# Kernel optimization log

Measured on AMD Instinct MI355X. Metric: run time of the kernel, lower is better.

## Reference

```python
import jax, jax.numpy as jnp
import numpy as np

K = 3
KV = K * K * K  # 27 kernel taps


def conv3d(x, w, b):
    # standard Conv3d, stride 1, padding 1 (the offset-predicting conv)
    out = jax.lax.conv_general_dilated(
        x, w, window_strides=(1, 1, 1), padding=[(1, 1), (1, 1), (1, 1)],
        dimension_numbers=('NCDHW', 'OIDHW', 'NCDHW'))
    return out + b[None, :, None, None, None]


def deform_conv3d_hw(x, offset, weight):
    # D3D deformable conv, dimension='HW': per kernel tap (kt,kh,kw) the sample
    # location gets fractional (dh,dw) offsets; t coordinate stays integer.
    B, C, T, H, W = x.shape
    Cout = weight.shape[0]
    off = offset.reshape(B, KV, 2, T, H, W)        # (dh, dw) per tap
    dh, dw = off[:, :, 0], off[:, :, 1]            # [B,KV,T,H,W]
    kt, kh, kw = jnp.meshgrid(jnp.arange(K), jnp.arange(K), jnp.arange(K), indexing='ij')
    kt, kh, kw = kt.reshape(KV), kh.reshape(KV), kw.reshape(KV)
    ti = jnp.arange(T)[None, :, None, None] + (kt - 1)[:, None, None, None]  # [KV,T,1,1] int
    hs = (jnp.arange(H)[None, None, :, None] + (kh - 1)[:, None, None, None]).astype(x.dtype) + dh
    ws = (jnp.arange(W)[None, None, None, :] + (kw - 1)[:, None, None, None]).astype(x.dtype) + dw
    tvalid = (ti >= 0) & (ti < T)                                # [KV,T,1,1]
    tic = jnp.broadcast_to(jnp.clip(ti, 0, T - 1), (KV, T, H, W))
    h0 = jnp.floor(hs).astype(jnp.int32); h1 = h0 + 1
    w0 = jnp.floor(ws).astype(jnp.int32); w1 = w0 + 1
    lh = hs - h0.astype(x.dtype)
    lw = ws - w0.astype(x.dtype)

    def sample(hi, wi):
        # bilinear corner gather with zero padding outside the volume
        m = (tvalid[None] & (hi >= 0) & (hi < H) & (wi >= 0) & (wi < W)).astype(x.dtype)
        hic = jnp.clip(hi, 0, H - 1)
        wic = jnp.clip(wi, 0, W - 1)
        def g(xb, hib, wib, mb):
            return xb[:, tic, hib, wib] * mb[None]   # [C,KV,T,H,W]
        return jax.vmap(g)(x, hic, wic, m)           # [B,C,KV,T,H,W]

    v00 = sample(h0, w0); v01 = sample(h0, w1)
    v10 = sample(h1, w0); v11 = sample(h1, w1)
    lh = lh[:, None]; lw = lw[:, None]               # broadcast over C
    cols = ((1 - lh) * (1 - lw) * v00 + (1 - lh) * lw * v01
            + lh * (1 - lw) * v10 + lh * lw * v11)   # [B,C,KV,T,H,W]
    return jnp.einsum('bckthw,ock->bothw', cols, weight.reshape(Cout, C, KV))


def leaky_relu(x):
    return jnp.where(x >= 0, x, 0.1 * x)


def setup_inputs() -> dict:
    key = jax.random.key(0)
    ks = jax.random.split(key, 6)
    B, C, T, H, W = 2, 64, 4, 64, 64
    OFF = 2 * KV  # 54 offset channels for dimension='HW'
    s = 1.0 / float(np.sqrt(C * KV))
    x = jax.random.normal(ks[0], (B, C, T, H, W), dtype=jnp.float32)
    dcn0_weight = jax.random.normal(ks[1], (C, C, K, K, K), jnp.float32) * s
    off0_weight = jax.random.normal(ks[2], (OFF, C, K, K, K), jnp.float32) * (0.02 * s)
    off0_bias = jnp.zeros((OFF,), jnp.float32)
    dcn1_weight = jax.random.normal(ks[3], (C, C, K, K, K), jnp.float32) * s
    off1_weight = jax.random.normal(ks[4], (OFF, C, K, K, K), jnp.float32) * (0.02 * s)
    off1_bias = jnp.zeros((OFF,), jnp.float32)
    return dict(x=x, dcn0_weight=dcn0_weight, off0_weight=off0_weight, off0_bias=off0_bias,
                dcn1_weight=dcn1_weight, off1_weight=off1_weight, off1_bias=off1_bias)


def reference(x, dcn0_weight, off0_weight, off0_bias, dcn1_weight, off1_weight, off1_bias):
    y = deform_conv3d_hw(x, conv3d(x, off0_weight, off0_bias), dcn0_weight)
    y = leaky_relu(y)
    return deform_conv3d_hw(y, conv3d(y, off1_weight, off1_bias), dcn1_weight) + x
```

## Files before the change

### kernel.cpp

```cpp
#include <hip/hip_runtime.h>
#include <hip/hip_bf16.h>

#define DEVI __device__ __forceinline__

constexpr int Bc = 2, Cc = 64, Tc = 4, Hc = 64, Wc = 64, OFFc = 54, KVc = 27;
constexpr int HW  = Hc * Wc;
constexpr int THW = Tc * HW;

typedef __attribute__((ext_vector_type(8))) short bf16x8;
typedef __attribute__((ext_vector_type(4))) float f32x4;

DEVI short f2bf(float f) {
    __hip_bfloat16 h = __float2bfloat16(f);
    return *reinterpret_cast<short*>(&h);
}
DEVI float bf2f(short s) {
    unsigned u = ((unsigned)(unsigned short)s) << 16;
    float f; __builtin_memcpy(&f, &u, 4); return f;
}

__global__ __launch_bounds__(256) void w_prep4(
    const float* __restrict__ w0, const float* __restrict__ w1,
    const float* __restrict__ w2, const float* __restrict__ w3,
    __hip_bfloat16* __restrict__ d0, __hip_bfloat16* __restrict__ d1,
    __hip_bfloat16* __restrict__ d2, __hip_bfloat16* __restrict__ d3)
{
    int gi = blockIdx.x;
    int seg = gi / 432;
    int i = (gi - seg * 432) * 256 + threadIdx.x;
    if (i >= 216 * 512) return;
    const float* w = seg == 0 ? w0 : seg == 1 ? w1 : seg == 2 ? w2 : w3;
    __hip_bfloat16* dst = seg == 0 ? d0 : seg == 1 ? d1 : seg == 2 ? d2 : d3;
    int ovalid = (seg < 2) ? OFFc : Cc;
    int u = i >> 9, r = i & 511;
    int mf = u & 3, ch = (u >> 2) & 1, tap = u >> 3;
    int o = mf * 16 + (r >> 5), c = ch * 32 + (r & 31);
    float v = (o < ovalid) ? w[(o * Cc + c) * KVc + tap] : 0.f;
    dst[i] = __float2bfloat16(v);
}

__global__ __launch_bounds__(256) void cast_cl(const float* __restrict__ x,
                                               __hip_bfloat16* __restrict__ xcl) {
    __shared__ float s[64][65];
    int tid = threadIdx.x;
    int bi  = blockIdx.x;
    int h = bi & 63, t = (bi >> 6) & 3, b = bi >> 8;

    const float* xp = x + (size_t)b * Cc * THW + t * HW + h * 64;
    int w0 = tid & 63, c0 = tid >> 6;
    #pragma unroll
    for (int i = 0; i < 16; ++i) {
        int c = c0 + i * 4;
        s[c][w0] = xp[(size_t)c * THW + w0];
    }
    __syncthreads();

    __hip_bfloat16* dst = xcl + (((size_t)b * Tc + t) * HW + (size_t)h * 64) * 64;
    #pragma unroll
    for (int r = 0; r < 2; ++r) {
        int j  = tid + r * 256;
        int w  = j >> 3;
        int c8 = j & 7;
        bf16x8 v;
        #pragma unroll
        for (int jj = 0; jj < 8; ++jj)
            v[jj] = f2bf(s[c8 * 8 + jj][w]);
        *reinterpret_cast<bf16x8*>(dst + w * 64 + c8 * 8) = v;
    }
}

constexpr int WT = 40;
constexpr int RSTRIDE = WT * 128;
constexpr int OFFB = 14256;

template <bool L2>
__global__ __launch_bounds__(512, 2) void fused_deform(
    const __hip_bfloat16* __restrict__ src, const __hip_bfloat16* __restrict__ owAk,
    const float* __restrict__ obias, const __hip_bfloat16* __restrict__ wAk,
    const float* __restrict__ xres, float* __restrict__ outf,
    __hip_bfloat16* __restrict__ ycl)
{
    __shared__ __align__(16) char s_mem[6 * RSTRIDE + 2 * OFFB];
    short* s_tile = (short*)s_mem;
    float* sp0    = (float*)(s_mem + 6 * RSTRIDE);
    float* sp1    = (float*)(s_mem + 6 * RSTRIDE + OFFB);
    float* s_off  = sp0;
    float* red0 = (float*)s_mem;
    float* red1 = (float*)s_mem + 64 * 68;

    int tid = threadIdx.x;
    int wv = tid >> 6, lane = tid & 63, l15 = lane & 15, l4 = lane >> 4;
    int nf = wv & 3, chh = wv >> 2;

    int bi = blockIdx.x;
    int xcd = bi & 7, idx = bi >> 3;
    int jgrp = xcd >> 1, whalf = xcd & 1;
    int b = jgrp >> 1;
    int h2 = idx & 31;
    int tsel = (idx >> 5) & 1;
    int t = ((jgrp & 1) << 1) + tsel;
    int h0 = h2 * 2;
    int wb = whalf * 32;

    int pl = nf * 16 + l15;
    int prow = pl >> 5, pcol = pl & 31;
    int hr = h0 + prow;
    int p  = wb + pcol;
    int cbase = chh * 32 + l4 * 8;
    int ktlo = (t == 0) ? 1 : 0, kthi = (t == 3) ? 2 : 3;

    const __hip_bfloat16* xb = src + ((size_t)b << 20);

    auto stage = [&](int kt) {
        int tt = t + kt - 1;
        const __hip_bfloat16* xt = xb + ((size_t)tt << 18);
        for (int i = tid; i < 6 * WT * 8; i += 512) {
            int r = i / (WT * 8), v = i - r * (WT * 8);
            int wl = v >> 3, ss = v & 7;
            int hh = h0 - 2 + r;
            int wg = wb - 3 + wl;
            bf16x8 val = {0, 0, 0, 0, 0, 0, 0, 0};
            if ((unsigned)hh < 64u && (unsigned)wg < 64u)
                val = *reinterpret_cast<const bf16x8*>(xt + ((hh * 64 + wg) << 6) + ss * 8);
            int byte = (r * RSTRIDE + wl * 128 + ss * 16) ^ ((wl & 7) << 4);
            *reinterpret_cast<bf16x8*>((char*)s_tile + byte) = val;
        }
    };
    auto ldread = [&](int sl, int wg) -> bf16x8 {
        int wl = wg - (wb - 3);
        int byte = (sl * RSTRIDE + wl * 128 + cbase * 2) ^ ((wl & 7) << 4);
        return *reinterpret_cast<const bf16x8*>((const char*)s_tile + byte);
    };

    f32x4 cacc[4];
    #pragma unroll
    for (int mf = 0; mf < 4; ++mf) cacc[mf] = (f32x4){0.f, 0.f, 0.f, 0.f};

    for (int kt = ktlo; kt < kthi; ++kt) {
        __syncthreads();
        stage(kt);
        __syncthreads();
        #pragma clang loop unroll(disable)
        for (int rr = 0; rr < 9; ++rr) {
            int kh = rr / 3, kw = rr - kh * 3, tap = kt * 9 + rr;
            int ws = p + kw - 1;
            int wsc = min(max(ws, 0), 63);
            bf16x8 bv = ldread(prow + kh + 1, wsc);
            if ((unsigned)ws >= 64u) bv = (bf16x8){0, 0, 0, 0, 0, 0, 0, 0};
            const __hip_bfloat16* ab = owAk + ((tap * 2 + chh) << 11) + (l15 << 5) + (l4 << 3);
            #pragma unroll
            for (int mf = 0; mf < 4; ++mf) {
                bf16x8 af = *reinterpret_cast<const bf16x8*>(ab + (mf << 9));
                cacc[mf] = __builtin_amdgcn_mfma_f32_16x16x32_bf16(af, bv, cacc[mf], 0, 0, 0);
            }
        }
    }
    {
        float* sp = chh ? sp1 : sp0;
        #pragma unroll
        for (int mf = 0; mf < 4; ++mf)
            #pragma unroll
            for (int jj = 0; jj < 4; ++jj) {
                int o = mf * 16 + l4 * 4 + jj;
                if (o < OFFc) sp[(o >> 1) * 132 + (o & 1) * 66 + pl] = cacc[mf][jj];
            }
    }
    __syncthreads();
    for (int i = tid; i < KVc * 2 * 66; i += 512) {
        int k = i / 132, rem = i - k * 132, jo = rem / 66;
        sp0[i] = sp0[i] + sp1[i] + obias[2 * k + jo];
    }

    f32x4 dacc[4];
    #pragma unroll
    for (int mf = 0; mf < 4; ++mf) dacc[mf] = (f32x4){0.f, 0.f, 0.f, 0.f};

    unsigned badmask = 0;

    for (int kt = kthi - 1; kt >= ktlo; --kt) {
        __syncthreads();
        if (kt != kthi - 1) {
            stage(kt);
            __syncthreads();
        }
        #pragma clang loop unroll_count(2)
        for (int rr = 0; rr < 9; ++rr) {
            int kh = rr / 3, kw = rr - kh * 3, tap = kt * 9 + rr;
            float dh = s_off[tap * 132 + pl];
            float dw = s_off[tap * 132 + 66 + pl];
            float hs  = (float)(hr + kh - 1) + dh;
            float wsf = (float)(p + kw - 1) + dw;
            float fh = floorf(hs), fw = floorf(wsf);
            int hfl = (int)fh, w0 = (int)fw;
            float lh = hs - fh, lw = wsf - fw;
            float q0 = (1.f - lw) * (((unsigned)w0 < 64u) ? 1.f : 0.f);
            float q1 = lw         * (((unsigned)(w0 + 1) < 64u) ? 1.f : 0.f);
            int wc0 = min(max(w0, 0), 63), wc1 = min(max(w0 + 1, 0), 63);
            int r0 = hfl - (h0 - 2);
            int r0c = min(max(r0, 0), 4);
            badmask |= ((r0 != r0c) ? 1u : 0u) << tap;
            bf16x8 g0 = ldread(r0c, wc0),     g1 = ldread(r0c, wc1);
            bf16x8 g2 = ldread(r0c + 1, wc0), g3 = ldread(r0c + 1, wc1);
            float cf0 = (1.f - lh) * q0, cf1 = (1.f - lh) * q1;
            float cf2 = lh * q0,         cf3 = lh * q1;
            bf16x8 bfrag;
            #pragma unroll
            for (int jj = 0; jj < 8; ++jj) {
                float s = cf0 * bf2f(g0[jj]) + cf1 * bf2f(g1[jj])
                        + cf2 * bf2f(g2[jj]) + cf3 * bf2f(g3[jj]);
                bfrag[jj] = f2bf(s);
            }
            const __hip_bfloat16* ab = wAk + ((tap * 2 + chh) << 11) + (l15 << 5) + (l4 << 3);
            #pragma unroll
            for (int mf = 0; mf < 4; ++mf) {
                bf16x8 af = *reinterpret_cast<const bf16x8*>(ab + (mf << 9));
                dacc[mf] = __builtin_amdgcn_mfma_f32_16x16x32_bf16(af, bfrag, dacc[mf], 0, 0, 0);
            }
        }
    }

    if (__any((int)(badmask != 0u))) {
        for (int kt = ktlo; kt < kthi; ++kt) {
            int tt = t + kt - 1;
            const __hip_bfloat16* xt = xb + ((size_t)tt << 18);
            #pragma clang loop unroll(disable)
            for (int rr = 0; rr < 9; ++rr) {
                int tap = kt * 9 + rr;
                if (!__any((int)((badmask >> tap) & 1u))) continue;
                int kh = rr / 3, kw = rr - kh * 3;
                float dh = s_off[tap * 132 + pl];
                float dw = s_off[tap * 132 + 66 + pl];
                float hs  = (float)(hr + kh - 1) + dh;
                float wsf = (float)(p + kw - 1) + dw;
                float fh = floorf(hs), fw = floorf(wsf);
                int hfl = (int)fh, w0 = (int)fw;
                float lh = hs - fh, lw = wsf - fw;
                float q0 = (1.f - lw) * (((unsigned)w0 < 64u) ? 1.f : 0.f);
                float q1 = lw         * (((unsigned)(w0 + 1) < 64u) ? 1.f : 0.f);
                int wc0 = min(max(w0, 0), 63), wc1 = min(max(w0 + 1, 0), 63);
                int r0 = hfl - (h0 - 2);
                int r0c = min(max(r0, 0), 4);
                bool bad = ((badmask >> tap) & 1u) != 0u;
                float u0 = (1.f - lh) * (((unsigned)hfl < 64u) ? 1.f : 0.f);
                float u1 = lh         * (((unsigned)(hfl + 1) < 64u) ? 1.f : 0.f);
                int hc0 = min(max(hfl, 0), 63), hc1 = min(max(hfl + 1, 0), 63);
                bf16x8 tg0 = *reinterpret_cast<const bf16x8*>(xt + ((hc0 * 64 + wc0) << 6) + cbase);
                bf16x8 tg1 = *reinterpret_cast<const bf16x8*>(xt + ((hc0 * 64 + wc1) << 6) + cbase);
                bf16x8 tg2 = *reinterpret_cast<const bf16x8*>(xt + ((hc1 * 64 + wc0) << 6) + cbase);
                bf16x8 tg3 = *reinterpret_cast<const bf16x8*>(xt + ((hc1 * 64 + wc1) << 6) + cbase);
                int ra0 = h0 - 2 + r0c, ra1 = ra0 + 1;
                float m0 = ((unsigned)ra0 < 64u) ? 1.f : 0.f;
                float m1 = ((unsigned)ra1 < 64u) ? 1.f : 0.f;
                int rc0 = min(max(ra0, 0), 63), rc1 = min(max(ra1, 0), 63);
                bf16x8 ag0 = *reinterpret_cast<const bf16x8*>(xt + ((rc0 * 64 + wc0) << 6) + cbase);
                bf16x8 ag1 = *reinterpret_cast<const bf16x8*>(xt + ((rc0 * 64 + wc1) << 6) + cbase);
                bf16x8 ag2 = *reinterpret_cast<const bf16x8*>(xt + ((rc1 * 64 + wc0) << 6) + cbase);
                bf16x8 ag3 = *reinterpret_cast<const bf16x8*>(xt + ((rc1 * 64 + wc1) << 6) + cbase);
                bf16x8 bfrag;
                #pragma unroll
                for (int jj = 0; jj < 8; ++jj) {
                    float ft = u0 * (q0 * bf2f(tg0[jj]) + q1 * bf2f(tg1[jj]))
                             + u1 * (q0 * bf2f(tg2[jj]) + q1 * bf2f(tg3[jj]));
                    float fa = (1.f - lh) * m0 * (q0 * bf2f(ag0[jj]) + q1 * bf2f(ag1[jj]))
                             + lh * m1 * (q0 * bf2f(ag2[jj]) + q1 * bf2f(ag3[jj]));
                    bfrag[jj] = f2bf(bad ? (ft - fa) : 0.f);
                }
                const __hip_bfloat16* ab = wAk + ((tap * 2 + chh) << 11) + (l15 << 5) + (l4 << 3);
                #pragma unroll
                for (int mf = 0; mf < 4; ++mf) {
                    bf16x8 af = *reinterpret_cast<const bf16x8*>(ab + (mf << 9));
                    dacc[mf] = __builtin_amdgcn_mfma_f32_16x16x32_bf16(af, bfrag, dacc[mf], 0, 0, 0);
                }
            }
        }
    }

    __syncthreads();
    {
        float* red = chh ? red1 : red0;
        #pragma unroll
        for (int mf = 0; mf < 4; ++mf)
            #pragma unroll
            for (int jj = 0; jj < 4; ++jj) {
                int o = mf * 16 + l4 * 4 + jj;
                red[pl * 68 + o] = dacc[mf][jj];
            }
    }
    __syncthreads();

    if (!L2) {
        int pp = tid >> 3, o8 = (tid & 7) << 3;
        int er = pp >> 5, ew = pp & 31;
        __hip_bfloat16* dst = ycl + ((((size_t)b * Tc + t) * HW + (h0 + er) * 64 + wb + ew) << 6) + o8;
        bf16x8 o8v;
        #pragma unroll
        for (int jj = 0; jj < 8; ++jj) {
            int i = pp * 68 + o8 + jj;
            float v = red0[i] + red1[i];
            v = v >= 0.f ? v : 0.1f * v;
            o8v[jj] = f2bf(v);
        }
        *reinterpret_cast<bf16x8*>(dst) = o8v;
    } else {
        int o = tid >> 3, pg = (tid & 7) << 3;
        int er = pg >> 5, ew = pg & 31;
        size_t base = ((size_t)(b * Cc + o) * Tc + t) * HW + (h0 + er) * 64 + wb + ew;
        #pragma unroll
        for (int q = 0; q < 2; ++q) {
            f32x4 r, xv = *reinterpret_cast<const f32x4*>(xres + base + q * 4);
            #pragma unroll
            for (int jj = 0; jj < 4; ++jj) {
                int i = (pg + q * 4 + jj) * 68 + o;
                r[jj] = red0[i] + red1[i] + xv[jj];
            }
            *reinterpret_cast<f32x4*>(outf + base + q * 4) = r;
        }
    }
}

extern "C" void kernel_launch(void* const* d_in, const int* in_sizes, int n_in,
                              void* d_out, int out_size, void* d_ws, size_t ws_size,
                              hipStream_t stream)
{
    const float* x   = (const float*)d_in[0];
    const float* w0  = (const float*)d_in[1];
    const float* ow0 = (const float*)d_in[2];
    const float* ob0 = (const float*)d_in[3];
    const float* w1  = (const float*)d_in[4];
    const float* ow1 = (const float*)d_in[5];
    const float* ob1 = (const float*)d_in[6];
    float* out = (float*)d_out;

    __hip_bfloat16* xcl  = (__hip_bfloat16*)d_ws;
    __hip_bfloat16* ycl  = xcl  + (size_t)Bc * THW * 64;
    __hip_bfloat16* owA0 = ycl  + (size_t)Bc * THW * 64;
    __hip_bfloat16* owA1 = owA0 + (size_t)216 * 512;
    __hip_bfloat16* wA0  = owA1 + (size_t)216 * 512;
    __hip_bfloat16* wA1  = wA0  + (size_t)216 * 512;

    w_prep4<<<1728, 256, 0, stream>>>(ow0, ow1, w0, w1, owA0, owA1, wA0, wA1);
    cast_cl<<<512, 256, 0, stream>>>(x, xcl);

    fused_deform<false><<<512, 512, 0, stream>>>(xcl, owA0, ob0, wA0, nullptr, nullptr, ycl);
    fused_deform<true><<<512, 512, 0, stream>>>(ycl, owA1, ob1, wA1, x, out, nullptr);
}
```

Baseline: 114.8 us.

## Split kernel taps across wave halves instead of input-channel halves

The two wave groups in each block used to split the 64 input channels into halves and run all 9 taps per kt. Now each group takes alternating taps and covers both channel halves per tap. This halves the per-wave offset reads, floor/bilinear-weight math and loop overhead for the deformable sampling, at the cost of double the LDS gathers and MFMAs per iteration with more registers live. The offset scatter layout is changed to keep the results consistent, and the reduction stores and reads are vectorised to f32x4.

Measured after the change: 141.8 us. 23.5% more time.

```diff
diff --git a/kernel.cpp b/kernel.cpp
--- a/kernel.cpp
+++ b/kernel.cpp
@@ -90,7 +90,7 @@
 
     int tid = threadIdx.x;
     int wv = tid >> 6, lane = tid & 63, l15 = lane & 15, l4 = lane >> 4;
-    int nf = wv & 3, chh = wv >> 2;
+    int nf = wv & 3, th = wv >> 2;
 
     int bi = blockIdx.x;
     int xcd = bi & 7, idx = bi >> 3;
@@ -106,7 +106,7 @@
     int prow = pl >> 5, pcol = pl & 31;
     int hr = h0 + prow;
     int p  = wb + pcol;
-    int cbase = chh * 32 + l4 * 8;
+    int cb0 = l4 * 8, cb1 = 32 + l4 * 8;
     int ktlo = (t == 0) ? 1 : 0, kthi = (t == 3) ? 2 : 3;
 
     const __hip_bfloat16* xb = src + ((size_t)b << 20);
@@ -126,9 +126,9 @@
             *reinterpret_cast<bf16x8*>((char*)s_tile + byte) = val;
         }
     };
-    auto ldread = [&](int sl, int wg) -> bf16x8 {
+    auto ldread = [&](int sl, int wg, int cb) -> bf16x8 {
         int wl = wg - (wb - 3);
-        int byte = (sl * RSTRIDE + wl * 128 + cbase * 2) ^ ((wl & 7) << 4);
+        int byte = (sl * RSTRIDE + wl * 128 + cb * 2) ^ ((wl & 7) << 4);
         return *reinterpret_cast<const bf16x8*>((const char*)s_tile + byte);
     };
 
@@ -140,29 +140,37 @@
         __syncthreads();
         stage(kt);
         __syncthreads();
+        int rr0 = (th + kt) & 1;
         #pragma clang loop unroll(disable)
-        for (int rr = 0; rr < 9; ++rr) {
+        for (int rr = rr0; rr < 9; rr += 2) {
             int kh = rr / 3, kw = rr - kh * 3, tap = kt * 9 + rr;
             int ws = p + kw - 1;
             int wsc = min(max(ws, 0), 63);
-            bf16x8 bv = ldread(prow + kh + 1, wsc);
-            if ((unsigned)ws >= 64u) bv = (bf16x8){0, 0, 0, 0, 0, 0, 0, 0};
-            const __hip_bfloat16* ab = owAk + ((tap * 2 + chh) << 11) + (l15 << 5) + (l4 << 3);
+            bf16x8 bv0 = ldread(prow + kh + 1, wsc, cb0);
+            bf16x8 bv1 = ldread(prow + kh + 1, wsc, cb1);
+            if ((unsigned)ws >= 64u) {
+                bv0 = (bf16x8){0, 0, 0, 0, 0, 0, 0, 0};
+                bv1 = (bf16x8){0, 0, 0, 0, 0, 0, 0, 0};
+            }
+            const __hip_bfloat16* ab0 = owAk + ((tap * 2 + 0) << 11) + (l15 << 5) + (l4 << 3);
+            const __hip_bfloat16* ab1 = owAk + ((tap * 2 + 1) << 11) + (l15 << 5) + (l4 << 3);
             #pragma unroll
             for (int mf = 0; mf < 4; ++mf) {
-                bf16x8 af = *reinterpret_cast<const bf16x8*>(ab + (mf << 9));
-                cacc[mf] = __builtin_amdgcn_mfma_f32_16x16x32_bf16(af, bv, cacc[mf], 0, 0, 0);
+                bf16x8 af0 = *reinterpret_cast<const bf16x8*>(ab0 + (mf << 9));
+                bf16x8 af1 = *reinterpret_cast<const bf16x8*>(ab1 + (mf << 9));
+                cacc[mf] = __builtin_amdgcn_mfma_f32_16x16x32_bf16(af0, bv0, cacc[mf], 0, 0, 0);
+                cacc[mf] = __builtin_amdgcn_mfma_f32_16x16x32_bf16(af1, bv1, cacc[mf], 0, 0, 0);
             }
         }
     }
     {
-        float* sp = chh ? sp1 : sp0;
+        float* sp = th ? sp1 : sp0;
         #pragma unroll
         for (int mf = 0; mf < 4; ++mf)
             #pragma unroll
             for (int jj = 0; jj < 4; ++jj) {
                 int o = mf * 16 + l4 * 4 + jj;
-                if (o < OFFc) sp[(o >> 1) * 132 + (o & 1) * 66 + pl] = cacc[mf][jj];
+                if (o < OFFc) sp[o * 66 + pl] = cacc[mf][jj];
             }
     }
     __syncthreads();
@@ -183,8 +191,9 @@
             stage(kt);
             __syncthreads();
         }
-        #pragma clang loop unroll_count(2)
-        for (int rr = 0; rr < 9; ++rr) {
+        int rr0 = (th + kt) & 1;
+        #pragma clang loop unroll(disable)
+        for (int rr = rr0; rr < 9; rr += 2) {
             int kh = rr / 3, kw = rr - kh * 3, tap = kt * 9 + rr;
             float dh = s_off[tap * 132 + pl];
             float dw = s_off[tap * 132 + 66 + pl];
@@ -199,22 +208,30 @@
             int r0 = hfl - (h0 - 2);
             int r0c = min(max(r0, 0), 4);
             badmask |= ((r0 != r0c) ? 1u : 0u) << tap;
-            bf16x8 g0 = ldread(r0c, wc0),     g1 = ldread(r0c, wc1);
-            bf16x8 g2 = ldread(r0c + 1, wc0), g3 = ldread(r0c + 1, wc1);
+            bf16x8 g0a = ldread(r0c, wc0, cb0),     g0b = ldread(r0c, wc0, cb1);
+            bf16x8 g1a = ldread(r0c, wc1, cb0),     g1b = ldread(r0c, wc1, cb1);
+            bf16x8 g2a = ldread(r0c + 1, wc0, cb0), g2b = ldread(r0c + 1, wc0, cb1);
+            bf16x8 g3a = ldread(r0c + 1, wc1, cb0), g3b = ldread(r0c + 1, wc1, cb1);
             float cf0 = (1.f - lh) * q0, cf1 = (1.f - lh) * q1;
             float cf2 = lh * q0,         cf3 = lh * q1;
-            bf16x8 bfrag;
+            bf16x8 bfr0, bfr1;
             #pragma unroll
             for (int jj = 0; jj < 8; ++jj) {
-                float s = cf0 * bf2f(g0[jj]) + cf1 * bf2f(g1[jj])
-                        + cf2 * bf2f(g2[jj]) + cf3 * bf2f(g3[jj]);
-                bfrag[jj] = f2bf(s);
-            }
-            const __hip_bfloat16* ab = wAk + ((tap * 2 + chh) << 11) + (l15 << 5) + (l4 << 3);
+                float s0 = cf0 * bf2f(g0a[jj]) + cf1 * bf2f(g1a[jj])
+                         + cf2 * bf2f(g2a[jj]) + cf3 * bf2f(g3a[jj]);
+                float s1 = cf0 * bf2f(g0b[jj]) + cf1 * bf2f(g1b[jj])
+                         + cf2 * bf2f(g2b[jj]) + cf3 * bf2f(g3b[jj]);
+                bfr0[jj] = f2bf(s0);
+                bfr1[jj] = f2bf(s1);
+            }
+            const __hip_bfloat16* ab0 = wAk + ((tap * 2 + 0) << 11) + (l15 << 5) + (l4 << 3);
+            const __hip_bfloat16* ab1 = wAk + ((tap * 2 + 1) << 11) + (l15 << 5) + (l4 << 3);
             #pragma unroll
             for (int mf = 0; mf < 4; ++mf) {
-                bf16x8 af = *reinterpret_cast<const bf16x8*>(ab + (mf << 9));
-                dacc[mf] = __builtin_amdgcn_mfma_f32_16x16x32_bf16(af, bfrag, dacc[mf], 0, 0, 0);
+                bf16x8 af0 = *reinterpret_cast<const bf16x8*>(ab0 + (mf << 9));
+                bf16x8 af1 = *reinterpret_cast<const bf16x8*>(ab1 + (mf << 9));
+                dacc[mf] = __builtin_amdgcn_mfma_f32_16x16x32_bf16(af0, bfr0, dacc[mf], 0, 0, 0);
+                dacc[mf] = __builtin_amdgcn_mfma_f32_16x16x32_bf16(af1, bfr1, dacc[mf], 0, 0, 0);
             }
         }
     }
@@ -223,8 +240,9 @@
         for (int kt = ktlo; kt < kthi; ++kt) {
             int tt = t + kt - 1;
             const __hip_bfloat16* xt = xb + ((size_t)tt << 18);
+            int rr0 = (th + kt) & 1;
             #pragma clang loop unroll(disable)
-            for (int rr = 0; rr < 9; ++rr) {
+            for (int rr = rr0; rr < 9; rr += 2) {
                 int tap = kt * 9 + rr;
                 if (!__any((int)((badmask >> tap) & 1u))) continue;
                 int kh = rr / 3, kw = rr - kh * 3;
@@ -244,32 +262,36 @@
                 float u0 = (1.f - lh) * (((unsigned)hfl < 64u) ? 1.f : 0.f);
                 float u1 = lh         * (((unsigned)(hfl + 1) < 64u) ? 1.f : 0.f);
                 int hc0 = min(max(hfl, 0), 63), hc1 = min(max(hfl + 1, 0), 63);
-                bf16x8 tg0 = *reinterpret_cast<const bf16x8*>(xt + ((hc0 * 64 + wc0) << 6) + cbase);
-                bf16x8 tg1 = *reinterpret_cast<const bf16x8*>(xt + ((hc0 * 64 + wc1) << 6) + cbase);
-                bf16x8 tg2 = *reinterpret_cast<const bf16x8*>(xt + ((hc1 * 64 + wc0) << 6) + cbase);
-                bf16x8 tg3 = *reinterpret_cast<const bf16x8*>(xt + ((hc1 * 64 + wc1) << 6) + cbase);
                 int ra0 = h0 - 2 + r0c, ra1 = ra0 + 1;
                 float m0 = ((unsigned)ra0 < 64u) ? 1.f : 0.f;
                 float m1 = ((unsigned)ra1 < 64u) ? 1.f : 0.f;
                 int rc0 = min(max(ra0, 0), 63), rc1 = min(max(ra1, 0), 63);
-                bf16x8 ag0 = *reinterpret_cast<const bf16x8*>(xt + ((rc0 * 64 + wc0) << 6) + cbase);
-                bf16x8 ag1 = *reinterpret_cast<const bf16x8*>(xt + ((rc0 * 64 + wc1) << 6) + cbase);
-                bf16x8 ag2 = *reinterpret_cast<const bf16x8*>(xt + ((rc1 * 64 + wc0) << 6) + cbase);
-                bf16x8 ag3 = *reinterpret_cast<const bf16x8*>(xt + ((rc1 * 64 + wc1) << 6) + cbase);
-                bf16x8 bfrag;
                 #pragma unroll
-                for (int jj = 0; jj < 8; ++jj) {
-                    float ft = u0 * (q0 * bf2f(tg0[jj]) + q1 * bf2f(tg1[jj]))
-                             + u1 * (q0 * bf2f(tg2[jj]) + q1 * bf2f(tg3[jj]));
-                    float fa = (1.f - lh) * m0 * (q0 * bf2f(ag0[jj]) + q1 * bf2f(ag1[jj]))
-                             + lh * m1 * (q0 * bf2f(ag2[jj]) + q1 * bf2f(ag3[jj]));
-                    bfrag[jj] = f2bf(bad ? (ft - fa) : 0.f);
-                }
-                const __hip_bfloat16* ab = wAk + ((tap * 2 + chh) << 11) + (l15 << 5) + (l4 << 3);
-                #pragma unroll
-                for (int mf = 0; mf < 4; ++mf) {
-                    bf16x8 af = *reinterpret_cast<const bf16x8*>(ab + (mf << 9));
-                    dacc[mf] = __builtin_amdgcn_mfma_f32_16x16x32_bf16(af, bfrag, dacc[mf], 0, 0, 0);
+                for (int half = 0; half < 2; ++half) {
+                    int cb = half ? cb1 : cb0;
+                    bf16x8 tg0 = *reinterpret_cast<const bf16x8*>(xt + ((hc0 * 64 + wc0) << 6) + cb);
+                    bf16x8 tg1 = *reinterpret_cast<const bf16x8*>(xt + ((hc0 * 64 + wc1) << 6) + cb);
+                    bf16x8 tg2 = *reinterpret_cast<const bf16x8*>(xt + ((hc1 * 64 + wc0) << 6) + cb);
+                    bf16x8 tg3 = *reinterpret_cast<const bf16x8*>(xt + ((hc1 * 64 + wc1) << 6) + cb);
+                    bf16x8 ag0 = *reinterpret_cast<const bf16x8*>(xt + ((rc0 * 64 + wc0) << 6) + cb);
+                    bf16x8 ag1 = *reinterpret_cast<const bf16x8*>(xt + ((rc0 * 64 + wc1) << 6) + cb);
+                    bf16x8 ag2 = *reinterpret_cast<const bf16x8*>(xt + ((rc1 * 64 + wc0) << 6) + cb);
+                    bf16x8 ag3 = *reinterpret_cast<const bf16x8*>(xt + ((rc1 * 64 + wc1) << 6) + cb);
+                    bf16x8 bfrag;
+                    #pragma unroll
+                    for (int jj = 0; jj < 8; ++jj) {
+                        float ft = u0 * (q0 * bf2f(tg0[jj]) + q1 * bf2f(tg1[jj]))
+                                 + u1 * (q0 * bf2f(tg2[jj]) + q1 * bf2f(tg3[jj]));
+                        float fa = (1.f - lh) * m0 * (q0 * bf2f(ag0[jj]) + q1 * bf2f(ag1[jj]))
+                                 + lh * m1 * (q0 * bf2f(ag2[jj]) + q1 * bf2f(ag3[jj]));
+                        bfrag[jj] = f2bf(bad ? (ft - fa) : 0.f);
+                    }
+                    const __hip_bfloat16* ab = wAk + ((tap * 2 + half) << 11) + (l15 << 5) + (l4 << 3);
+                    #pragma unroll
+                    for (int mf = 0; mf < 4; ++mf) {
+                        bf16x8 af = *reinterpret_cast<const bf16x8*>(ab + (mf << 9));
+                        dacc[mf] = __builtin_amdgcn_mfma_f32_16x16x32_bf16(af, bfrag, dacc[mf], 0, 0, 0);
+                    }
                 }
             }
         }
@@ -277,14 +299,10 @@
 
     __syncthreads();
     {
-        float* red = chh ? red1 : red0;
+        float* red = th ? red1 : red0;
         #pragma unroll
         for (int mf = 0; mf < 4; ++mf)
-            #pragma unroll
-            for (int jj = 0; jj < 4; ++jj) {
-                int o = mf * 16 + l4 * 4 + jj;
-                red[pl * 68 + o] = dacc[mf][jj];
-            }
+            *reinterpret_cast<f32x4*>(&red[pl * 68 + mf * 16 + l4 * 4]) = dacc[mf];
     }
     __syncthreads();
 
@@ -294,11 +312,15 @@
         __hip_bfloat16* dst = ycl + ((((size_t)b * Tc + t) * HW + (h0 + er) * 64 + wb + ew) << 6) + o8;
         bf16x8 o8v;
         #pragma unroll
-        for (int jj = 0; jj < 8; ++jj) {
-            int i = pp * 68 + o8 + jj;
-            float v = red0[i] + red1[i];
-            v = v >= 0.f ? v : 0.1f * v;
-            o8v[jj] = f2bf(v);
+        for (int q = 0; q < 2; ++q) {
+            f32x4 v0 = *reinterpret_cast<const f32x4*>(&red0[pp * 68 + o8 + q * 4]);
+            f32x4 v1 = *reinterpret_cast<const f32x4*>(&red1[pp * 68 + o8 + q * 4]);
+            #pragma unroll
+            for (int jj = 0; jj < 4; ++jj) {
+                float v = v0[jj] + v1[jj];
+                v = v >= 0.f ? v : 0.1f * v;
+                o8v[q * 4 + jj] = f2bf(v);
+            }
         }
         *reinterpret_cast<bf16x8*>(dst) = o8v;
     } else {
```
